# Optimization experiments

Measured on AMD Instinct MI355X. Metric: run time of the kernel, lower is better.

The kernel has to match this reference:

```python
import jax, jax.numpy as jnp
import numpy as np

EPS = 1e-8
NMS_K = 15          # soft_nms_3d window
COM_NMS = 7.0       # soft_nms_3d com_strength
COM_SCORE = 100.0   # score_com_strength
COM_SCALE = 100.0   # scale_com_strength


def conv2d(x, w, b=None, pad=1, groups=1):
    y = jax.lax.conv_general_dilated(
        x, w, (1, 1), [(pad, pad), (pad, pad)],
        dimension_numbers=('NCHW', 'OIHW', 'NCHW'),
        feature_group_count=groups)
    if b is not None:
        y = y + b[None, :, None, None]
    return y


def bn(x, s, b):  # folded inference batchnorm: scale + shift per channel
    return x * s[None, :, None, None] + b[None, :, None, None]


def maxpool_same(x, k):
    p = k // 2
    return jax.lax.reduce_window(x, -jnp.inf, jax.lax.max,
                                 (1, 1, k, k), (1, 1, 1, 1),
                                 [(0, 0), (0, 0), (p, p), (p, p)])


def boxsum_same(x, k):
    p = k // 2
    return jax.lax.reduce_window(x, 0.0, jax.lax.add,
                                 (1, 1, k, k), (1, 1, 1, 1),
                                 [(0, 0), (0, 0), (p, p), (p, p)])


def instance_norm(x, eps=1e-5):  # no affine (nn.InstanceNorm2d default)
    mu = x.mean(axis=(2, 3), keepdims=True)
    var = x.var(axis=(2, 3), keepdims=True)
    return (x - mu) * jax.lax.rsqrt(var + eps)


def inverted_residual(x, dw_w, bna_s, bna_b, pw_w, bnb_s, bnb_b):
    # expand_ratio=1, stride=1, inp==oup -> residual connection
    h = conv2d(x, dw_w, pad=1, groups=x.shape[1])
    h = jnp.clip(bn(h, bna_s, bna_b), 0.0, 6.0)       # ReLU6
    h = conv2d(h, pw_w, pad=0)
    h = bn(h, bnb_s, bnb_b)
    return x + h


def forward(photos, w0, b0, dw1_w, bn1a_s, bn1a_b, pw1_w, bn1b_s, bn1b_b,
            dw2_w, bn2a_s, bn2a_b, pw2_w, bn2b_s, bn2b_b, ws, bs, scale_list):
    x = conv2d(photos, w0, b0)                                   # (B,16,H,W)
    x = inverted_residual(x, dw1_w, bn1a_s, bn1a_b, pw1_w, bn1b_s, bn1b_b)
    x = inverted_residual(x, dw2_w, bn2a_s, bn2a_b, pw2_w, bn2b_s, bn2b_b)
    s = conv2d(x, ws, bs)                                        # (B,C,H,W) C=scales
    s = jax.nn.leaky_relu(instance_norm(s), negative_slope=0.01)

    # ---- soft_nms_3d: windowed competitive softmax over (scale, 15x15) ----
    m = maxpool_same(s, NMS_K).max(axis=1, keepdims=True)        # (B,1,H,W)
    e = jnp.exp(COM_NMS * (s - m))                               # (B,C,H,W)
    sum_e = boxsum_same(e.sum(axis=1, keepdims=True), NMS_K)     # (B,1,H,W)
    probs = e / (sum_e + EPS)                                    # (B,C,H,W)

    # ---- soft_max_and_argmax_1d over scale dim ----
    mx = probs.max(axis=1, keepdims=True)
    e1 = jnp.exp(COM_SCORE * (probs - mx))
    p1 = e1 / (e1.sum(axis=1, keepdims=True) + EPS)
    e2 = jnp.exp(COM_SCALE * (probs - mx))
    p2 = e2 / (e2.sum(axis=1, keepdims=True) + EPS)
    score_map = (probs * p1).sum(axis=1, keepdims=True)          # (B,1,H,W)
    scale_map = (scale_list[None, :, None, None] * p2).sum(axis=1, keepdims=True)
    # return channel-last like the torch code (B,H,W,1)
    return (score_map.transpose(0, 2, 3, 1), scale_map.transpose(0, 2, 3, 1))


def setup_inputs() -> dict:
    key = jax.random.key(0)
    ks = jax.random.split(key, 20)
    B, H, W, C, S = 4, 512, 512, 16, 10
    rn = lambda k, sh, sc=0.1: (jax.random.normal(k, sh, jnp.float32) * sc)
    inp = {
        'photos': jax.random.normal(ks[0], (B, 1, H, W), jnp.float32),
        'w0': rn(ks[1], (C, 1, 3, 3)), 'b0': rn(ks[2], (C,)),
        'dw1_w': rn(ks[3], (C, 1, 3, 3)),
        'bn1a_s': jax.random.uniform(ks[4], (C,), jnp.float32, 0.5, 1.5),
        'bn1a_b': rn(ks[5], (C,)),
        'pw1_w': rn(ks[6], (C, C, 1, 1)),
        'bn1b_s': jax.random.uniform(ks[7], (C,), jnp.float32, 0.5, 1.5),
        'bn1b_b': rn(ks[8], (C,)),
        'dw2_w': rn(ks[9], (C, 1, 3, 3)),
        'bn2a_s': jax.random.uniform(ks[10], (C,), jnp.float32, 0.5, 1.5),
        'bn2a_b': rn(ks[11], (C,)),
        'pw2_w': rn(ks[12], (C, C, 1, 1)),
        'bn2b_s': jax.random.uniform(ks[13], (C,), jnp.float32, 0.5, 1.5),
        'bn2b_b': rn(ks[14], (C,)),
        'ws': rn(ks[15], (S, C, 3, 3)), 'bs': rn(ks[16], (S,)),
        'scale_list': jnp.linspace(3.0, 21.0, S, dtype=jnp.float32),
    }
    return inp


def reference(photos, w0, b0, dw1_w, bn1a_s, bn1a_b, pw1_w, bn1b_s, bn1b_b,
              dw2_w, bn2a_s, bn2a_b, pw2_w, bn2b_s, bn2b_b, ws, bs, scale_list):
    return forward(photos, w0, b0, dw1_w, bn1a_s, bn1a_b, pw1_w, bn1b_s, bn1b_b,
                   dw2_w, bn2a_s, bn2a_b, pw2_w, bn2b_s, bn2b_b, ws, bs, scale_list)
```

## Files before the change

kernel.cpp:

```cpp
#include <hip/hip_runtime.h>
#include <hip/hip_bf16.h>

#define Bn 4
#define Hn 512
#define Wn 512
#define Cn 16
#define Sn 10
#define HWn (Hn*Wn)
#define BHW (Bn*HWn)
#define NG (BHW/4)

__device__ __forceinline__ void load_row6(const float* __restrict__ rp, bool valid,
                                          int w0, float* r) {
    if (valid) {
        float4 v = *reinterpret_cast<const float4*>(rp + w0);
        r[1] = v.x; r[2] = v.y; r[3] = v.z; r[4] = v.w;
        r[0] = (w0 > 0)   ? rp[w0 - 1] : 0.f;
        r[5] = (w0 < 508) ? rp[w0 + 4] : 0.f;
    } else {
        r[0] = r[1] = r[2] = r[3] = r[4] = r[5] = 0.f;
    }
}

__global__ __launch_bounds__(256) void k_conv0(const float* __restrict__ photos,
        const float* __restrict__ w0v, const float* __restrict__ b0,
        float* __restrict__ out) {
    __shared__ float wp[Cn*12];
    __shared__ float sb[Cn];
    int t = threadIdx.x;
    if (t < Cn*9) { int o = t / 9, k = t % 9; wp[o*12 + k] = w0v[t]; }
    if (t < Cn) sb[t] = b0[t];
    __syncthreads();
    int idx = blockIdx.x * 256 + t;
    int w0 = (idx & 127) << 2, h = (idx >> 7) & 511, b = idx >> 16;
    const float* pb = photos + (b << 18);
    float xr[3][6];
    #pragma unroll
    for (int dy = 0; dy < 3; ++dy) {
        int hh = h + dy - 1;
        load_row6(pb + (hh << 9), (unsigned)hh < 512u, w0, xr[dy]);
    }
    #pragma unroll
    for (int o = 0; o < Cn; ++o) {
        float4 wa = *(const float4*)&wp[o*12];
        float4 wb = *(const float4*)&wp[o*12 + 4];
        float wk8 = wp[o*12 + 8];
        float wk[9] = {wa.x, wa.y, wa.z, wa.w, wb.x, wb.y, wb.z, wb.w, wk8};
        float bv = sb[o];
        float a0 = bv, a1 = bv, a2 = bv, a3 = bv;
        #pragma unroll
        for (int dy = 0; dy < 3; ++dy)
            #pragma unroll
            for (int dx = 0; dx < 3; ++dx) {
                float wv = wk[dy*3 + dx];
                a0 += xr[dy][dx + 0] * wv;
                a1 += xr[dy][dx + 1] * wv;
                a2 += xr[dy][dx + 2] * wv;
                a3 += xr[dy][dx + 3] * wv;
            }
        float4 r; r.x = a0; r.y = a1; r.z = a2; r.w = a3;
        *reinterpret_cast<float4*>(out + ((b*Cn + o) << 18) + (h << 9) + w0) = r;
    }
}

#define IR_COMPUTE(cc, xr) do {                                                 \
    const int c_ = (cc);                                                        \
    float4 wa_ = *(const float4*)&dwp[c_*12];                                   \
    float4 wb_ = *(const float4*)&dwp[c_*12 + 4];                               \
    float wk8_ = dwp[c_*12 + 8];                                                \
    float wk_[9] = {wa_.x, wa_.y, wa_.z, wa_.w, wb_.x, wb_.y, wb_.z, wb_.w, wk8_}; \
    float t0 = 0.f, t1 = 0.f, t2 = 0.f, t3 = 0.f;                               \
    _Pragma("unroll")                                                           \
    for (int dy = 0; dy < 3; ++dy) {                                            \
        _Pragma("unroll")                                                       \
        for (int dx = 0; dx < 3; ++dx) {                                        \
            float wv = wk_[dy*3 + dx];                                          \
            t0 += xr[dy][dx + 0] * wv;                                          \
            t1 += xr[dy][dx + 1] * wv;                                          \
            t2 += xr[dy][dx + 2] * wv;                                          \
            t3 += xr[dy][dx + 3] * wv;                                          \
        }                                                                       \
    }                                                                           \
    float sc_ = sas[c_], sh_ = sab[c_];                                         \
    t0 = fminf(fmaxf(t0*sc_ + sh_, 0.f), 6.f);                                  \
    t1 = fminf(fmaxf(t1*sc_ + sh_, 0.f), 6.f);                                  \
    t2 = fminf(fmaxf(t2*sc_ + sh_, 0.f), 6.f);                                  \
    t3 = fminf(fmaxf(t3*sc_ + sh_, 0.f), 6.f);                                  \
    _Pragma("unroll")                                                           \
    for (int o4 = 0; o4 < 4; ++o4) {                                            \
        float4 wq = *(const float4*)&pwT[c_*16 + o4*4];                         \
        acc[o4*4+0][0] += t0*wq.x; acc[o4*4+0][1] += t1*wq.x;                   \
        acc[o4*4+0][2] += t2*wq.x; acc[o4*4+0][3] += t3*wq.x;                   \
        acc[o4*4+1][0] += t0*wq.y; acc[o4*4+1][1] += t1*wq.y;                   \
        acc[o4*4+1][2] += t2*wq.y; acc[o4*4+1][3] += t3*wq.y;                   \
        acc[o4*4+2][0] += t0*wq.z; acc[o4*4+2][1] += t1*wq.z;                   \
        acc[o4*4+2][2] += t2*wq.z; acc[o4*4+2][3] += t3*wq.z;                   \
        acc[o4*4+3][0] += t0*wq.w; acc[o4*4+3][1] += t1*wq.w;                   \
        acc[o4*4+3][2] += t2*wq.w; acc[o4*4+3][3] += t3*wq.w;                   \
    }                                                                           \
} while (0)

__global__ __launch_bounds__(256) void k_ir(const float* __restrict__ x,
        float* __restrict__ y, const float* __restrict__ dww,
        const float* __restrict__ as_, const float* __restrict__ ab_,
        const float* __restrict__ pww, const float* __restrict__ bs_,
        const float* __restrict__ bb_) {
    __shared__ float dwp[Cn*12];
    __shared__ float pwT[Cn*Cn];
    __shared__ float sas[Cn], sab[Cn], sbs[Cn], sbb[Cn];
    int t = threadIdx.x;
    if (t < Cn*9)  { int c = t / 9, k = t % 9; dwp[c*12 + k] = dww[t]; }
    if (t < Cn*Cn) { int o = t >> 4, i = t & 15; pwT[i*16 + o] = pww[t]; }
    if (t < Cn) { sas[t] = as_[t]; sab[t] = ab_[t]; sbs[t] = bs_[t]; sbb[t] = bb_[t]; }
    __syncthreads();
    int idx = blockIdx.x * 256 + t;
    int w0 = (idx & 127) << 2, h = (idx >> 7) & 511, b = idx >> 16;
    const float* xb = x + ((size_t)b << 22);
    float acc[Cn][4];
    #pragma unroll
    for (int o = 0; o < Cn; ++o) { acc[o][0] = acc[o][1] = acc[o][2] = acc[o][3] = 0.f; }
    float xrA[3][6], xrB[3][6];
    #pragma unroll
    for (int dy = 0; dy < 3; ++dy) {
        int hh = h + dy - 1;
        load_row6(xb + (hh << 9), (unsigned)hh < 512u, w0, xrA[dy]);
    }
    #pragma unroll 1
    for (int c = 0; c < Cn; c += 2) {
        #pragma unroll
        for (int dy = 0; dy < 3; ++dy) {
            int hh = h + dy - 1;
            load_row6(xb + ((c + 1) << 18) + (hh << 9), (unsigned)hh < 512u, w0, xrB[dy]);
        }
        IR_COMPUTE(c, xrA);
        if (c + 2 < Cn) {
            #pragma unroll
            for (int dy = 0; dy < 3; ++dy) {
                int hh = h + dy - 1;
                load_row6(xb + ((c + 2) << 18) + (hh << 9), (unsigned)hh < 512u, w0, xrA[dy]);
            }
        }
        IR_COMPUTE(c + 1, xrB);
    }
    #pragma unroll
    for (int o = 0; o < Cn; ++o) {
        const float* xo = xb + (o << 18) + (h << 9) + w0;
        float4 xv = *(const float4*)xo;
        float sc = sbs[o], sh = sbb[o];
        float4 r;
        r.x = xv.x + acc[o][0]*sc + sh;
        r.y = xv.y + acc[o][1]*sc + sh;
        r.z = xv.z + acc[o][2]*sc + sh;
        r.w = xv.w + acc[o][3]*sc + sh;
        *reinterpret_cast<float4*>(y + ((size_t)b << 22) + (o << 18) + (h << 9) + w0) = r;
    }
}

#define CONVS_COMPUTE(cc, xr) do {                                              \
    const int c_ = (cc);                                                        \
    _Pragma("unroll")                                                           \
    for (int o = 0; o < Sn; ++o) {                                              \
        const float* wb_ = &wp[(c_*Sn + o)*12];                                 \
        float4 wa_ = *(const float4*)wb_;                                       \
        float4 wv_ = *(const float4*)(wb_ + 4);                                 \
        float wk8_ = wb_[8];                                                    \
        float wk_[9] = {wa_.x, wa_.y, wa_.z, wa_.w, wv_.x, wv_.y, wv_.z, wv_.w, wk8_}; \
        _Pragma("unroll")                                                       \
        for (int dy = 0; dy < 3; ++dy) {                                        \
            _Pragma("unroll")                                                   \
            for (int dx = 0; dx < 3; ++dx) {                                    \
                float wv = wk_[dy*3 + dx];                                      \
                acc[o][0] += xr[dy][dx + 0] * wv;                               \
                acc[o][1] += xr[dy][dx + 1] * wv;                               \
                acc[o][2] += xr[dy][dx + 2] * wv;                               \
                acc[o][3] += xr[dy][dx + 3] * wv;                               \
            }                                                                   \
        }                                                                       \
    }                                                                           \
} while (0)

__global__ __launch_bounds__(256) void k_convs(const float* __restrict__ x,
        const float* __restrict__ wsw, const float* __restrict__ bsv,
        float* __restrict__ s) {
    __shared__ float wp[Cn*Sn*12];
    __shared__ float sb[Sn];
    int t = threadIdx.x;
    for (int i = t; i < Sn*Cn*9; i += 256) {
        int o = i / (Cn*9), r = i % (Cn*9), c = r / 9, k = r % 9;
        wp[(c*Sn + o)*12 + k] = wsw[i];
    }
    if (t < Sn) sb[t] = bsv[t];
    __syncthreads();
    int idx = blockIdx.x * 256 + t;
    int w0 = (idx & 127) << 2, h = (idx >> 7) & 511, b = idx >> 16;
    const float* xb = x + ((size_t)b << 22);
    float acc[Sn][4];
    #pragma unroll
    for (int o = 0; o < Sn; ++o) {
        float bv = sb[o];
        acc[o][0] = bv; acc[o][1] = bv; acc[o][2] = bv; acc[o][3] = bv;
    }
    float xrA[3][6], xrB[3][6];
    #pragma unroll
    for (int dy = 0; dy < 3; ++dy) {
        int hh = h + dy - 1;
        load_row6(xb + (hh << 9), (unsigned)hh < 512u, w0, xrA[dy]);
    }
    #pragma unroll 1
    for (int c = 0; c < Cn; c += 2) {
        #pragma unroll
        for (int dy = 0; dy < 3; ++dy) {
            int hh = h + dy - 1;
            load_row6(xb + ((c + 1) << 18) + (hh << 9), (unsigned)hh < 512u, w0, xrB[dy]);
        }
        CONVS_COMPUTE(c, xrA);
        if (c + 2 < Cn) {
            #pragma unroll
            for (int dy = 0; dy < 3; ++dy) {
                int hh = h + dy - 1;
                load_row6(xb + ((c + 2) << 18) + (hh << 9), (unsigned)hh < 512u, w0, xrA[dy]);
            }
        }
        CONVS_COMPUTE(c + 1, xrB);
    }
    #pragma unroll
    for (int o = 0; o < Sn; ++o) {
        float4 r; r.x = acc[o][0]; r.y = acc[o][1]; r.z = acc[o][2]; r.w = acc[o][3];
        *reinterpret_cast<float4*>(s + ((b*Sn + o) << 18) + (h << 9) + w0) = r;
    }
}

__global__ __launch_bounds__(256) void k_in_part(const float* __restrict__ s,
                                                 double* __restrict__ part) {
    int bc = blockIdx.x >> 5, ch = blockIdx.x & 31;
    const float4* p4 = (const float4*)(s + ((size_t)bc << 18) + (ch << 13));
    int t = threadIdx.x;
    double sum = 0.0, sq = 0.0;
    #pragma unroll
    for (int i = 0; i < 8; ++i) {
        float4 v = p4[t + i * 256];
        sum += (double)v.x + (double)v.y + (double)v.z + (double)v.w;
        sq  += (double)v.x*v.x + (double)v.y*v.y + (double)v.z*v.z + (double)v.w*v.w;
    }
    __shared__ double ssum[256], ssq[256];
    ssum[t] = sum; ssq[t] = sq;
    __syncthreads();
    for (int off = 128; off > 0; off >>= 1) {
        if (t < off) { ssum[t] += ssum[t + off]; ssq[t] += ssq[t + off]; }
        __syncthreads();
    }
    if (t == 0) {
        part[blockIdx.x * 2]     = ssum[0];
        part[blockIdx.x * 2 + 1] = ssq[0];
    }
}

__global__ __launch_bounds__(64) void k_in_fin(const double* __restrict__ part,
                                               float2* __restrict__ stats) {
    int bc = blockIdx.x;
    int t = threadIdx.x;
    double sum = 0.0, sq = 0.0;
    if (t < 32) { sum = part[(bc * 32 + t) * 2]; sq = part[(bc * 32 + t) * 2 + 1]; }
    #pragma unroll
    for (int off = 32; off > 0; off >>= 1) {
        sum += __shfl_xor(sum, off);
        sq  += __shfl_xor(sq, off);
    }
    if (t == 0) {
        double mu = sum / (double)HWn;
        double var = sq / (double)HWn - mu * mu;
        float2 st; st.x = (float)mu; st.y = rsqrtf((float)var + 1e-5f);
        stats[bc] = st;
    }
}

__device__ __forceinline__ float nrm(float v, float2 st) {
    float r = (v - st.x) * st.y;
    return r >= 0.f ? r : 0.01f * r;
}

__global__ __launch_bounds__(256) void k_chan_rowmax(const float* __restrict__ s,
        const float2* __restrict__ stats, float* __restrict__ m1) {
    __shared__ float rowbuf[512];
    int bh = blockIdx.x;
    int b = bh >> 9, h = bh & 511;
    int t = threadIdx.x, w0 = t << 1;
    const float* sp = s + ((size_t)(b * Sn) << 18) + (h << 9) + w0;
    float mx0 = -INFINITY, mx1 = -INFINITY;
    #pragma unroll
    for (int c = 0; c < Sn; ++c) {
        float2 st = stats[b * Sn + c];
        float2 v = *reinterpret_cast<const float2*>(sp + ((size_t)c << 18));
        mx0 = fmaxf(mx0, nrm(v.x, st));
        mx1 = fmaxf(mx1, nrm(v.y, st));
    }
    rowbuf[w0] = mx0; rowbuf[w0 + 1] = mx1;
    __syncthreads();
    float2 o;
    {
        int lo = max(w0 - 7, 0), hi = min(w0 + 7, 511);
        float m = -INFINITY;
        for (int ww = lo; ww <= hi; ++ww) m = fmaxf(m, rowbuf[ww]);
        o.x = m;
        int w1 = w0 + 1;
        lo = max(w1 - 7, 0); hi = min(w1 + 7, 511);
        m = -INFINITY;
        for (int ww = lo; ww <= hi; ++ww) m = fmaxf(m, rowbuf[ww]);
        o.y = m;
    }
    *reinterpret_cast<float2*>(m1 + (bh << 9) + w0) = o;
}

__global__ __launch_bounds__(256) void k_col_expsum(const float* __restrict__ s,
        const float2* __restrict__ stats, const float* __restrict__ m1,
        float* __restrict__ mfull, float* __restrict__ tout) {
    __shared__ float esbuf[512];
    int bh = blockIdx.x;
    int b = bh >> 9, h = bh & 511;
    int t = threadIdx.x, w0 = t << 1;
    int lo = max(h - 7, 0), hi = min(h + 7, 511);
    float2 m = make_float2(-INFINITY, -INFINITY);
    for (int hh = lo; hh <= hi; ++hh) {
        float2 v = *reinterpret_cast<const float2*>(m1 + ((size_t)b << 18) + (hh << 9) + w0);
        m.x = fmaxf(m.x, v.x); m.y = fmaxf(m.y, v.y);
    }
    *reinterpret_cast<float2*>(mfull + (bh << 9) + w0) = m;
    const float* sp = s + ((size_t)(b * Sn) << 18) + (h << 9) + w0;
    float es0 = 0.f, es1 = 0.f;
    #pragma unroll
    for (int c = 0; c < Sn; ++c) {
        float2 st = stats[b * Sn + c];
        float2 v = *reinterpret_cast<const float2*>(sp + ((size_t)c << 18));
        es0 += __expf(7.f * (nrm(v.x, st) - m.x));
        es1 += __expf(7.f * (nrm(v.y, st) - m.y));
    }
    esbuf[w0] = es0; esbuf[w0 + 1] = es1;
    __syncthreads();
    float2 o;
    {
        int wlo = max(w0 - 7, 0), whi = min(w0 + 7, 511);
        float a = 0.f;
        for (int ww = wlo; ww <= whi; ++ww) a += esbuf[ww];
        o.x = a;
        int w1 = w0 + 1;
        wlo = max(w1 - 7, 0); whi = min(w1 + 7, 511);
        a = 0.f;
        for (int ww = wlo; ww <= whi; ++ww) a += esbuf[ww];
        o.y = a;
    }
    *reinterpret_cast<float2*>(tout + (bh << 9) + w0) = o;
}

__global__ __launch_bounds__(256) void k_final(const float* __restrict__ s,
        const float2* __restrict__ stats, const float* __restrict__ mfull,
        const float* __restrict__ tin, const float* __restrict__ scl,
        float* __restrict__ out) {
    __shared__ float sscale[Sn];
    int t = threadIdx.x;
    if (t < Sn) sscale[t] = scl[t];
    __syncthreads();
    int bh = blockIdx.x;
    int b = bh >> 9, h = bh & 511;
    int w0 = t << 1;
    int lo = max(h - 7, 0), hi = min(h + 7, 511);
    float2 su = make_float2(0.f, 0.f);
    for (int hh = lo; hh <= hi; ++hh) {
        float2 v = *reinterpret_cast<const float2*>(tin + ((size_t)b << 18) + (hh << 9) + w0);
        su.x += v.x; su.y += v.y;
    }
    float2 m = *reinterpret_cast<const float2*>(mfull + (bh << 9) + w0);
    float d0 = 1.f / (su.x + 1e-8f), d1i = 1.f / (su.y + 1e-8f);
    const float* sp = s + ((size_t)(b * Sn) << 18) + (h << 9) + w0;
    float pr0[Sn], pr1[Sn];
    float mx0 = -INFINITY, mx1 = -INFINITY;
    #pragma unroll
    for (int c = 0; c < Sn; ++c) {
        float2 st = stats[b * Sn + c];
        float2 v = *reinterpret_cast<const float2*>(sp + ((size_t)c << 18));
        float p0 = expf(7.f * (nrm(v.x, st) - m.x)) * d0;
        float p1 = expf(7.f * (nrm(v.y, st) - m.y)) * d1i;
        pr0[c] = p0; pr1[c] = p1;
        mx0 = fmaxf(mx0, p0); mx1 = fmaxf(mx1, p1);
    }
    float e0[Sn], e1[Sn];
    float s0 = 0.f, s1 = 0.f;
    #pragma unroll
    for (int c = 0; c < Sn; ++c) {
        e0[c] = expf(100.f * (pr0[c] - mx0)); s0 += e0[c];
        e1[c] = expf(100.f * (pr1[c] - mx1)); s1 += e1[c];
    }
    float i0 = 1.f / (s0 + 1e-8f), i1 = 1.f / (s1 + 1e-8f);
    float sc0 = 0.f, sc1 = 0.f, sl0 = 0.f, sl1 = 0.f;
    #pragma unroll
    for (int c = 0; c < Sn; ++c) {
        float p0 = e0[c] * i0, p1 = e1[c] * i1;
        sc0 += pr0[c] * p0; sl0 += sscale[c] * p0;
        sc1 += pr1[c] * p1; sl1 += sscale[c] * p1;
    }
    int oi = (bh << 9) + w0;
    float2 r0; r0.x = sc0; r0.y = sc1;
    float2 r1; r1.x = sl0; r1.y = sl1;
    *reinterpret_cast<float2*>(out + oi) = r0;
    *reinterpret_cast<float2*>(out + BHW + oi) = r1;
}

extern "C" void kernel_launch(void* const* d_in, const int* in_sizes, int n_in,
                              void* d_out, int out_size, void* d_ws, size_t ws_size,
                              hipStream_t stream) {
    const float* photos = (const float*)d_in[0];
    const float* w0     = (const float*)d_in[1];
    const float* b0     = (const float*)d_in[2];
    const float* dw1_w  = (const float*)d_in[3];
    const float* bn1a_s = (const float*)d_in[4];
    const float* bn1a_b = (const float*)d_in[5];
    const float* pw1_w  = (const float*)d_in[6];
    const float* bn1b_s = (const float*)d_in[7];
    const float* bn1b_b = (const float*)d_in[8];
    const float* dw2_w  = (const float*)d_in[9];
    const float* bn2a_s = (const float*)d_in[10];
    const float* bn2a_b = (const float*)d_in[11];
    const float* pw2_w  = (const float*)d_in[12];
    const float* bn2b_s = (const float*)d_in[13];
    const float* bn2b_b = (const float*)d_in[14];
    const float* ws_w   = (const float*)d_in[15];
    const float* bs_v   = (const float*)d_in[16];
    const float* scl    = (const float*)d_in[17];

    char* wsb = (char*)d_ws;
    float* A  = (float*)(wsb);
    float* Bb = (float*)(wsb + 67108864);
    float* S  = (float*)(wsb + 134217728);
    float2* stats = (float2*)Bb;
    double* part  = (double*)(Bb + 1024);
    float* M1 = A;
    float* M  = A + 1 * (1 << 20);
    float* T  = A + 2 * (1 << 20);

    dim3 blk(256);
    int gNG  = NG / 256;
    int gROW = Bn * Hn;

    k_conv0<<<gNG, blk, 0, stream>>>(photos, w0, b0, A);
    k_ir<<<gNG, blk, 0, stream>>>(A, Bb, dw1_w, bn1a_s, bn1a_b, pw1_w, bn1b_s, bn1b_b);
    k_ir<<<gNG, blk, 0, stream>>>(Bb, A, dw2_w, bn2a_s, bn2a_b, pw2_w, bn2b_s, bn2b_b);
    k_convs<<<gNG, blk, 0, stream>>>(A, ws_w, bs_v, S);
    k_in_part<<<Bn * Sn * 32, blk, 0, stream>>>(S, part);
    k_in_fin<<<Bn * Sn, dim3(64), 0, stream>>>(part, stats);
    k_chan_rowmax<<<gROW, blk, 0, stream>>>(S, stats, M1);
    k_col_expsum<<<gROW, blk, 0, stream>>>(S, stats, M1, M, T);
    k_final<<<gROW, blk, 0, stream>>>(S, stats, M, T, scl, (float*)d_out);
}
```

Before: 232.1 us.

## Stage 3x3 conv input tiles in double-buffered LDS with shuffle halos

The depthwise/inverted-residual and scale-conv kernels now process an 8x128 spatial tile per block. Each input channel is loaded once into a double-buffered shared-memory tile (10 rows plus left/right halo columns), with the next channel prefetched into registers while the current one is computed. Horizontal neighbours come from warp shuffles instead of redundant global loads. This removes the roughly 3x redundant global row reads of the per-thread scheme, at the cost of a barrier per channel and extra LDS traffic.

```diff
diff --git a/kernel.cpp b/kernel.cpp
--- a/kernel.cpp
+++ b/kernel.cpp
@@ -63,88 +63,141 @@
     }
 }
 
-#define IR_COMPUTE(cc, xr) do {                                                 \
-    const int c_ = (cc);                                                        \
-    float4 wa_ = *(const float4*)&dwp[c_*12];                                   \
-    float4 wb_ = *(const float4*)&dwp[c_*12 + 4];                               \
-    float wk8_ = dwp[c_*12 + 8];                                                \
-    float wk_[9] = {wa_.x, wa_.y, wa_.z, wa_.w, wb_.x, wb_.y, wb_.z, wb_.w, wk8_}; \
-    float t0 = 0.f, t1 = 0.f, t2 = 0.f, t3 = 0.f;                               \
+
+struct StageRegs { float4 b0, b1; float hl, hr; };
+
+__device__ __forceinline__ StageRegs stage_load(const float* __restrict__ xc,
+                                                int w0, int h0, int t) {
+    StageRegs r;
+    {
+        int row = t >> 5, c4 = t & 31;
+        int gh = h0 - 1 + row;
+        r.b0 = make_float4(0.f, 0.f, 0.f, 0.f);
+        if ((unsigned)gh < 512u)
+            r.b0 = *reinterpret_cast<const float4*>(xc + (gh << 9) + w0 + (c4 << 2));
+    }
+    r.b1 = make_float4(0.f, 0.f, 0.f, 0.f);
+    if (t < 64) {
+        int s = t + 256;
+        int row = s >> 5, c4 = s & 31;
+        int gh = h0 - 1 + row;
+        if ((unsigned)gh < 512u)
+            r.b1 = *reinterpret_cast<const float4*>(xc + (gh << 9) + w0 + (c4 << 2));
+    }
+    r.hl = 0.f; r.hr = 0.f;
+    if (t < 10) {
+        int gh = h0 - 1 + t;
+        if (w0 > 0 && (unsigned)gh < 512u) r.hl = xc[(gh << 9) + w0 - 1];
+    }
+    if (t >= 32 && t < 42) {
+        int gh = h0 - 1 + (t - 32);
+        if (w0 + 128 < 512 && (unsigned)gh < 512u) r.hr = xc[(gh << 9) + w0 + 128];
+    }
+    return r;
+}
+
+__device__ __forceinline__ void stage_write(float (*tile)[128], float* hL, float* hR,
+                                            const StageRegs& r, int t) {
+    *reinterpret_cast<float4*>(&tile[t >> 5][(t & 31) << 2]) = r.b0;
+    if (t < 64) {
+        int s = t + 256;
+        *reinterpret_cast<float4*>(&tile[s >> 5][(s & 31) << 2]) = r.b1;
+    }
+    if (t < 10) hL[t] = r.hl;
+    if (t >= 32 && t < 42) hR[t - 32] = r.hr;
+}
+
+#define READ_ROWS(tilebuf, hLbuf, hRbuf)                                        \
+    float4 v_[3]; float lft_[3], rgt_[3];                                       \
     _Pragma("unroll")                                                           \
     for (int dy = 0; dy < 3; ++dy) {                                            \
-        _Pragma("unroll")                                                       \
-        for (int dx = 0; dx < 3; ++dx) {                                        \
-            float wv = wk_[dy*3 + dx];                                          \
-            t0 += xr[dy][dx + 0] * wv;                                          \
-            t1 += xr[dy][dx + 1] * wv;                                          \
-            t2 += xr[dy][dx + 2] * wv;                                          \
-            t3 += xr[dy][dx + 3] * wv;                                          \
-        }                                                                       \
-    }                                                                           \
-    float sc_ = sas[c_], sh_ = sab[c_];                                         \
-    t0 = fminf(fmaxf(t0*sc_ + sh_, 0.f), 6.f);                                  \
-    t1 = fminf(fmaxf(t1*sc_ + sh_, 0.f), 6.f);                                  \
-    t2 = fminf(fmaxf(t2*sc_ + sh_, 0.f), 6.f);                                  \
-    t3 = fminf(fmaxf(t3*sc_ + sh_, 0.f), 6.f);                                  \
-    _Pragma("unroll")                                                           \
-    for (int o4 = 0; o4 < 4; ++o4) {                                            \
-        float4 wq = *(const float4*)&pwT[c_*16 + o4*4];                         \
-        acc[o4*4+0][0] += t0*wq.x; acc[o4*4+0][1] += t1*wq.x;                   \
-        acc[o4*4+0][2] += t2*wq.x; acc[o4*4+0][3] += t3*wq.x;                   \
-        acc[o4*4+1][0] += t0*wq.y; acc[o4*4+1][1] += t1*wq.y;                   \
-        acc[o4*4+1][2] += t2*wq.y; acc[o4*4+1][3] += t3*wq.y;                   \
-        acc[o4*4+2][0] += t0*wq.z; acc[o4*4+2][1] += t1*wq.z;                   \
-        acc[o4*4+2][2] += t2*wq.z; acc[o4*4+2][3] += t3*wq.z;                   \
-        acc[o4*4+3][0] += t0*wq.w; acc[o4*4+3][1] += t1*wq.w;                   \
-        acc[o4*4+3][2] += t2*wq.w; acc[o4*4+3][3] += t3*wq.w;                   \
-    }                                                                           \
-} while (0)
+        v_[dy] = *reinterpret_cast<const float4*>(&(tilebuf)[th + dy][tw << 2]);\
+        float l_ = __shfl_up(v_[dy].w, 1);                                      \
+        if (tw == 0) l_ = (hLbuf)[th + dy];                                     \
+        float rr_ = __shfl_down(v_[dy].x, 1);                                   \
+        if (tw == 31) rr_ = (hRbuf)[th + dy];                                   \
+        lft_[dy] = l_; rgt_[dy] = rr_;                                          \
+    }
 
 __global__ __launch_bounds__(256) void k_ir(const float* __restrict__ x,
         float* __restrict__ y, const float* __restrict__ dww,
         const float* __restrict__ as_, const float* __restrict__ ab_,
         const float* __restrict__ pww, const float* __restrict__ bs_,
         const float* __restrict__ bb_) {
+    __shared__ float tile[2][10][128];
+    __shared__ float hLs[2][10], hRs[2][10];
     __shared__ float dwp[Cn*12];
     __shared__ float pwT[Cn*Cn];
     __shared__ float sas[Cn], sab[Cn], sbs[Cn], sbb[Cn];
     int t = threadIdx.x;
+    { int o = t >> 4, i = t & 15; pwT[i*16 + o] = pww[t]; }
     if (t < Cn*9)  { int c = t / 9, k = t % 9; dwp[c*12 + k] = dww[t]; }
-    if (t < Cn*Cn) { int o = t >> 4, i = t & 15; pwT[i*16 + o] = pww[t]; }
-    if (t < Cn) { sas[t] = as_[t]; sab[t] = ab_[t]; sbs[t] = bs_[t]; sbb[t] = bb_[t]; }
-    __syncthreads();
-    int idx = blockIdx.x * 256 + t;
-    int w0 = (idx & 127) << 2, h = (idx >> 7) & 511, b = idx >> 16;
+    if (t < Cn) { sas[t] = as_[t]; sab[t] = ab_[t]; }
+    if (t >= 64 && t < 64 + Cn) { sbs[t-64] = bs_[t-64]; sbb[t-64] = bb_[t-64]; }
+
+    int bx = blockIdx.x;
+    int wt = bx & 3, ht = (bx >> 2) & 63, b = bx >> 8;
+    int w0 = wt << 7, h0 = ht << 3;
+    int tw = t & 31, th = t >> 5;
     const float* xb = x + ((size_t)b << 22);
+
     float acc[Cn][4];
     #pragma unroll
     for (int o = 0; o < Cn; ++o) { acc[o][0] = acc[o][1] = acc[o][2] = acc[o][3] = 0.f; }
-    float xrA[3][6], xrB[3][6];
-    #pragma unroll
-    for (int dy = 0; dy < 3; ++dy) {
-        int hh = h + dy - 1;
-        load_row6(xb + (hh << 9), (unsigned)hh < 512u, w0, xrA[dy]);
-    }
+
+    StageRegs sr = stage_load(xb, w0, h0, t);
+    stage_write(tile[0], hLs[0], hRs[0], sr, t);
+    __syncthreads();
+
     #pragma unroll 1
-    for (int c = 0; c < Cn; c += 2) {
+    for (int c = 0; c < Cn; ++c) {
+        if (c + 1 < Cn) sr = stage_load(xb + ((c + 1) << 18), w0, h0, t);
+        int bf = c & 1;
+        READ_ROWS(tile[bf], hLs[bf], hRs[bf]);
+        float4 wa = *(const float4*)&dwp[c*12];
+        float4 wb = *(const float4*)&dwp[c*12 + 4];
+        float wk8 = dwp[c*12 + 8];
+        float wk[9] = {wa.x, wa.y, wa.z, wa.w, wb.x, wb.y, wb.z, wb.w, wk8};
+        float t0 = 0.f, t1 = 0.f, t2 = 0.f, t3 = 0.f;
         #pragma unroll
         for (int dy = 0; dy < 3; ++dy) {
-            int hh = h + dy - 1;
-            load_row6(xb + ((c + 1) << 18) + (hh << 9), (unsigned)hh < 512u, w0, xrB[dy]);
-        }
-        IR_COMPUTE(c, xrA);
-        if (c + 2 < Cn) {
+            float r6[6] = {lft_[dy], v_[dy].x, v_[dy].y, v_[dy].z, v_[dy].w, rgt_[dy]};
             #pragma unroll
-            for (int dy = 0; dy < 3; ++dy) {
-                int hh = h + dy - 1;
-                load_row6(xb + ((c + 2) << 18) + (hh << 9), (unsigned)hh < 512u, w0, xrA[dy]);
+            for (int dx = 0; dx < 3; ++dx) {
+                float wv = wk[dy*3 + dx];
+                t0 += r6[dx + 0] * wv;
+                t1 += r6[dx + 1] * wv;
+                t2 += r6[dx + 2] * wv;
+                t3 += r6[dx + 3] * wv;
             }
         }
-        IR_COMPUTE(c + 1, xrB);
-    }
+        float sc = sas[c], sh = sab[c];
+        t0 = fminf(fmaxf(t0*sc + sh, 0.f), 6.f);
+        t1 = fminf(fmaxf(t1*sc + sh, 0.f), 6.f);
+        t2 = fminf(fmaxf(t2*sc + sh, 0.f), 6.f);
+        t3 = fminf(fmaxf(t3*sc + sh, 0.f), 6.f);
+        #pragma unroll
+        for (int o4 = 0; o4 < 4; ++o4) {
+            float4 wq = *(const float4*)&pwT[c*16 + o4*4];
+            acc[o4*4+0][0] += t0*wq.x; acc[o4*4+0][1] += t1*wq.x;
+            acc[o4*4+0][2] += t2*wq.x; acc[o4*4+0][3] += t3*wq.x;
+            acc[o4*4+1][0] += t0*wq.y; acc[o4*4+1][1] += t1*wq.y;
+            acc[o4*4+1][2] += t2*wq.y; acc[o4*4+1][3] += t3*wq.y;
+            acc[o4*4+2][0] += t0*wq.z; acc[o4*4+2][1] += t1*wq.z;
+            acc[o4*4+2][2] += t2*wq.z; acc[o4*4+2][3] += t3*wq.z;
+            acc[o4*4+3][0] += t0*wq.w; acc[o4*4+3][1] += t1*wq.w;
+            acc[o4*4+3][2] += t2*wq.w; acc[o4*4+3][3] += t3*wq.w;
+        }
+        if (c + 1 < Cn) {
+            int nb = (c + 1) & 1;
+            stage_write(tile[nb], hLs[nb], hRs[nb], sr, t);
+            __syncthreads();
+        }
+    }
+    int h = h0 + th, wg = w0 + (tw << 2);
     #pragma unroll
     for (int o = 0; o < Cn; ++o) {
-        const float* xo = xb + (o << 18) + (h << 9) + w0;
+        const float* xo = xb + (o << 18) + (h << 9) + wg;
         float4 xv = *(const float4*)xo;
         float sc = sbs[o], sh = sbb[o];
         float4 r;
@@ -152,36 +205,15 @@
         r.y = xv.y + acc[o][1]*sc + sh;
         r.z = xv.z + acc[o][2]*sc + sh;
         r.w = xv.w + acc[o][3]*sc + sh;
-        *reinterpret_cast<float4*>(y + ((size_t)b << 22) + (o << 18) + (h << 9) + w0) = r;
-    }
-}
-
-#define CONVS_COMPUTE(cc, xr) do {                                              \
-    const int c_ = (cc);                                                        \
-    _Pragma("unroll")                                                           \
-    for (int o = 0; o < Sn; ++o) {                                              \
-        const float* wb_ = &wp[(c_*Sn + o)*12];                                 \
-        float4 wa_ = *(const float4*)wb_;                                       \
-        float4 wv_ = *(const float4*)(wb_ + 4);                                 \
-        float wk8_ = wb_[8];                                                    \
-        float wk_[9] = {wa_.x, wa_.y, wa_.z, wa_.w, wv_.x, wv_.y, wv_.z, wv_.w, wk8_}; \
-        _Pragma("unroll")                                                       \
-        for (int dy = 0; dy < 3; ++dy) {                                        \
-            _Pragma("unroll")                                                   \
-            for (int dx = 0; dx < 3; ++dx) {                                    \
-                float wv = wk_[dy*3 + dx];                                      \
-                acc[o][0] += xr[dy][dx + 0] * wv;                               \
-                acc[o][1] += xr[dy][dx + 1] * wv;                               \
-                acc[o][2] += xr[dy][dx + 2] * wv;                               \
-                acc[o][3] += xr[dy][dx + 3] * wv;                               \
-            }                                                                   \
-        }                                                                       \
-    }                                                                           \
-} while (0)
+        *reinterpret_cast<float4*>(y + ((size_t)b << 22) + (o << 18) + (h << 9) + wg) = r;
+    }
+}
 
 __global__ __launch_bounds__(256) void k_convs(const float* __restrict__ x,
         const float* __restrict__ wsw, const float* __restrict__ bsv,
         float* __restrict__ s) {
+    __shared__ float tile[2][10][128];
+    __shared__ float hLs[2][10], hRs[2][10];
     __shared__ float wp[Cn*Sn*12];
     __shared__ float sb[Sn];
     int t = threadIdx.x;
@@ -190,43 +222,60 @@
         wp[(c*Sn + o)*12 + k] = wsw[i];
     }
     if (t < Sn) sb[t] = bsv[t];
-    __syncthreads();
-    int idx = blockIdx.x * 256 + t;
-    int w0 = (idx & 127) << 2, h = (idx >> 7) & 511, b = idx >> 16;
+
+    int bx = blockIdx.x;
+    int wt = bx & 3, ht = (bx >> 2) & 63, b = bx >> 8;
+    int w0 = wt << 7, h0 = ht << 3;
+    int tw = t & 31, th = t >> 5;
     const float* xb = x + ((size_t)b << 22);
+
     float acc[Sn][4];
     #pragma unroll
     for (int o = 0; o < Sn; ++o) {
-        float bv = sb[o];
+        float bv = bsv[o];
         acc[o][0] = bv; acc[o][1] = bv; acc[o][2] = bv; acc[o][3] = bv;
     }
-    float xrA[3][6], xrB[3][6];
-    #pragma unroll
-    for (int dy = 0; dy < 3; ++dy) {
-        int hh = h + dy - 1;
-        load_row6(xb + (hh << 9), (unsigned)hh < 512u, w0, xrA[dy]);
-    }
+
+    StageRegs sr = stage_load(xb, w0, h0, t);
+    stage_write(tile[0], hLs[0], hRs[0], sr, t);
+    __syncthreads();
+
     #pragma unroll 1
-    for (int c = 0; c < Cn; c += 2) {
+    for (int c = 0; c < Cn; ++c) {
+        if (c + 1 < Cn) sr = stage_load(xb + ((c + 1) << 18), w0, h0, t);
+        int bf = c & 1;
+        READ_ROWS(tile[bf], hLs[bf], hRs[bf]);
         #pragma unroll
-        for (int dy = 0; dy < 3; ++dy) {
-            int hh = h + dy - 1;
-            load_row6(xb + ((c + 1) << 18) + (hh << 9), (unsigned)hh < 512u, w0, xrB[dy]);
-        }
-        CONVS_COMPUTE(c, xrA);
-        if (c + 2 < Cn) {
+        for (int o = 0; o < Sn; ++o) {
+            const float* wb_ = &wp[(c*Sn + o)*12];
+            float4 wa = *(const float4*)wb_;
+            float4 wv2 = *(const float4*)(wb_ + 4);
+            float wk8 = wb_[8];
+            float wk[9] = {wa.x, wa.y, wa.z, wa.w, wv2.x, wv2.y, wv2.z, wv2.w, wk8};
             #pragma unroll
             for (int dy = 0; dy < 3; ++dy) {
-                int hh = h + dy - 1;
-                load_row6(xb + ((c + 2) << 18) + (hh << 9), (unsigned)hh < 512u, w0, xrA[dy]);
+                float r6[6] = {lft_[dy], v_[dy].x, v_[dy].y, v_[dy].z, v_[dy].w, rgt_[dy]};
+                #pragma unroll
+                for (int dx = 0; dx < 3; ++dx) {
+                    float wv = wk[dy*3 + dx];
+                    acc[o][0] += r6[dx + 0] * wv;
+                    acc[o][1] += r6[dx + 1] * wv;
+                    acc[o][2] += r6[dx + 2] * wv;
+                    acc[o][3] += r6[dx + 3] * wv;
+                }
             }
         }
-        CONVS_COMPUTE(c + 1, xrB);
-    }
+        if (c + 1 < Cn) {
+            int nb = (c + 1) & 1;
+            stage_write(tile[nb], hLs[nb], hRs[nb], sr, t);
+            __syncthreads();
+        }
+    }
+    int h = h0 + th, wg = w0 + (tw << 2);
     #pragma unroll
     for (int o = 0; o < Sn; ++o) {
         float4 r; r.x = acc[o][0]; r.y = acc[o][1]; r.z = acc[o][2]; r.w = acc[o][3];
-        *reinterpret_cast<float4*>(s + ((b*Sn + o) << 18) + (h << 9) + w0) = r;
+        *reinterpret_cast<float4*>(s + ((b*Sn + o) << 18) + (h << 9) + wg) = r;
     }
 }
 
@@ -437,13 +486,14 @@
     float* T  = A + 2 * (1 << 20);
 
     dim3 blk(256);
-    int gNG  = NG / 256;
-    int gROW = Bn * Hn;
+    int gNG   = NG / 256;
+    int gTILE = 4 * 64 * Bn;
+    int gROW  = Bn * Hn;
 
     k_conv0<<<gNG, blk, 0, stream>>>(photos, w0, b0, A);
-    k_ir<<<gNG, blk, 0, stream>>>(A, Bb, dw1_w, bn1a_s, bn1a_b, pw1_w, bn1b_s, bn1b_b);
-    k_ir<<<gNG, blk, 0, stream>>>(Bb, A, dw2_w, bn2a_s, bn2a_b, pw2_w, bn2b_s, bn2b_b);
-    k_convs<<<gNG, blk, 0, stream>>>(A, ws_w, bs_v, S);
+    k_ir<<<gTILE, blk, 0, stream>>>(A, Bb, dw1_w, bn1a_s, bn1a_b, pw1_w, bn1b_s, bn1b_b);
+    k_ir<<<gTILE, blk, 0, stream>>>(Bb, A, dw2_w, bn2a_s, bn2a_b, pw2_w, bn2b_s, bn2b_b);
+    k_convs<<<gTILE, blk, 0, stream>>>(A, ws_w, bs_v, S);
     k_in_part<<<Bn * Sn * 32, blk, 0, stream>>>(S, part);
     k_in_fin<<<Bn * Sn, dim3(64), 0, stream>>>(part, stats);
     k_chan_rowmax<<<gROW, blk, 0, stream>>>(S, stats, M1);
```

Measured after the change: 215.4 us. -7.2%, faster.
